# Kernel tuning notes

Hardware: AMD Instinct MI355X
Metric: run time of the kernel (lower is better)

## Reference

```python
import jax, jax.numpy as jnp
import numpy as np

HIDDEN = 2048
HEADS = 16
HEAD_DIM = HIDDEN // HEADS
BATCH = 2
SEQ = 2048


def setup_inputs() -> dict:
    key = jax.random.key(0)
    ks = jax.random.split(key, 9)
    s = 0.02
    return {
        "x": jax.random.normal(ks[0], (BATCH, SEQ, HIDDEN), dtype=jnp.float32),
        "wq": jax.random.normal(ks[1], (HIDDEN, HIDDEN), dtype=jnp.float32) * s,
        "bq": jax.random.normal(ks[2], (HIDDEN,), dtype=jnp.float32) * s,
        "wk": jax.random.normal(ks[3], (HIDDEN, HIDDEN), dtype=jnp.float32) * s,
        "bk": jax.random.normal(ks[4], (HIDDEN,), dtype=jnp.float32) * s,
        "wv": jax.random.normal(ks[5], (HIDDEN, HIDDEN), dtype=jnp.float32) * s,
        "bv": jax.random.normal(ks[6], (HIDDEN,), dtype=jnp.float32) * s,
        "wo": jax.random.normal(ks[7], (HIDDEN, HIDDEN), dtype=jnp.float32) * s,
        "bo": jax.random.normal(ks[8], (HIDDEN,), dtype=jnp.float32) * s,
    }


def reference(x, wq, bq, wk, bk, wv, bv, wo, bo):
    B, S, _ = x.shape
    scale = jnp.sqrt(jnp.float32(HEAD_DIM))
    # torch Linear: y = x @ W.T + b
    def proj(w, b):
        return (x @ w.T + b).reshape(B, S, HEADS, HEAD_DIM).transpose(0, 2, 1, 3)
    q = proj(wq, bq)  # [B,H,S,D]
    k = proj(wk, bk)
    v = proj(wv, bv)
    scores = jnp.einsum("bhqd,bhkd->bhqk", q, k) / scale  # [B,H,S,S]
    probs = jax.nn.softmax(scores, axis=-1)
    ctx = jnp.einsum("bhqk,bhkd->bhqd", probs, v)  # [B,H,S,D]
    ctx = ctx.transpose(0, 2, 1, 3).reshape(B, S, HIDDEN)
    return ctx @ wo.T + bo
```

## Files before the change

kernel.cpp:

```cpp
#include <hip/hip_runtime.h>

typedef unsigned short u16;
typedef unsigned int   u32;
typedef float  f32x4   __attribute__((ext_vector_type(4)));
typedef __bf16 bf16x8  __attribute__((ext_vector_type(8)));
typedef u16    u16x8   __attribute__((ext_vector_type(8)));
typedef u16    u16x4   __attribute__((ext_vector_type(4)));
typedef u32    u32x2   __attribute__((ext_vector_type(2)));
typedef u32    u32x4   __attribute__((ext_vector_type(4)));

#define HIDDEN 2048
#define SEQ    2048
#define NHEADS 16
#define HD     128
#define BATCH  2
#define QSTR   4096

typedef const __attribute__((address_space(3))) u16* lptr;

__device__ __forceinline__ u16 f2bf(float f) {
  u32 u = __builtin_bit_cast(u32, f);
  u += 0x7FFFu + ((u >> 16) & 1u);
  return (u16)(u >> 16);
}
__device__ __forceinline__ u32 pk2(float a, float b) {
  __bf16 x = (__bf16)a, y = (__bf16)b;
  return (u32)__builtin_bit_cast(u16, x) | ((u32)__builtin_bit_cast(u16, y) << 16);
}
__device__ __forceinline__ bf16x8 ld_frag(const u16* p) {
  return __builtin_bit_cast(bf16x8, *(const u32x4*)p);
}
__device__ __forceinline__ void gload_lds16(const u16* g, u16* l) {
  __builtin_amdgcn_global_load_lds((const __attribute__((address_space(1))) u32*)g,
                                   (__attribute__((address_space(3))) u32*)l, 16, 0, 0);
}

#define DSR(dst, base, lit) \
  asm volatile("ds_read_b128 %0, %1 offset:" lit : "=v"(dst) : "v"(base))

#define MFMA16(d, a, b) d = __builtin_amdgcn_mfma_f32_16x16x32_bf16(a, b, d, 0, 0, 0)

__global__ __launch_bounds__(256) void cvt_kernel(const float* __restrict__ src,
                                                  u16* __restrict__ dst, int n4) {
  int stride = gridDim.x * blockDim.x;
  for (int i = blockIdx.x * blockDim.x + threadIdx.x; i < n4; i += stride) {
    f32x4 v = ((const f32x4*)src)[i];
    u16x4 o;
    o[0] = f2bf(v[0]); o[1] = f2bf(v[1]); o[2] = f2bf(v[2]); o[3] = f2bf(v[3]);
    *(u16x4*)(dst + (size_t)i * 4) = o;
  }
}

__global__ __launch_bounds__(256) void cvt4_kernel(
    const float* __restrict__ s0, const float* __restrict__ s1,
    const float* __restrict__ s2, const float* __restrict__ s3,
    u16* __restrict__ o0, u16* __restrict__ o1,
    u16* __restrict__ o2, u16* __restrict__ o3, int n4) {
  const float* src = (blockIdx.y == 0) ? s0 : (blockIdx.y == 1) ? s1 : (blockIdx.y == 2) ? s2 : s3;
  u16* dst = (blockIdx.y == 0) ? o0 : (blockIdx.y == 1) ? o1 : (blockIdx.y == 2) ? o2 : o3;
  int stride = gridDim.x * blockDim.x;
  for (int i = blockIdx.x * blockDim.x + threadIdx.x; i < n4; i += stride) {
    f32x4 v = ((const f32x4*)src)[i];
    u16x4 o;
    o[0] = f2bf(v[0]); o[1] = f2bf(v[1]); o[2] = f2bf(v[2]); o[3] = f2bf(v[3]);
    *(u16x4*)(dst + (size_t)i * 4) = o;
  }
}

__global__ __launch_bounds__(512, 2) void gemm_qkv(
    const u16* __restrict__ A, const u16* __restrict__ Bt,
    const float* __restrict__ bq, const float* __restrict__ bk,
    const float* __restrict__ bv,
    u16* __restrict__ qk, u16* __restrict__ vtb, float qscale)
{
  __shared__ __attribute__((aligned(16))) u16 As[2][16384];
  __shared__ __attribute__((aligned(16))) u16 Bs[2][12288];

  const int tid  = threadIdx.x;
  const int lane = tid & 63;
  const int wave = tid >> 6;
  const int l15  = lane & 15;
  const int g    = lane >> 4;
  const int wm   = wave >> 2;
  const int wn   = wave & 3;

  const int id  = blockIdx.x;
  const int xcd = id & 7;
  const int c   = id >> 3;
  const int tileN = (xcd * 4 + (c >> 4)) * 192;
  const int tileM = (c & 15) << 8;

  const int srow = tid >> 3;
  const int gch8 = ((tid & 7) ^ (srow & 7)) * 8;
  const u16* agp = A  + (size_t)(tileM + srow) * HIDDEN + gch8;
  const u16* bgp = Bt + (size_t)(tileN + srow) * HIDDEN + gch8;
  u16* asp = (u16*)&As[0][0] + tid * 8;
  u16* bsp = (u16*)&Bs[0][0] + tid * 8;

  auto stage = [&](int buf, int ko) {
    u16* ad = asp + buf * 16384;
    u16* bd = bsp + buf * 12288;
#pragma unroll
    for (int r = 0; r < 4; ++r)
      gload_lds16(agp + (size_t)r * 64 * HIDDEN + ko, ad + r * 4096);
#pragma unroll
    for (int r = 0; r < 3; ++r)
      gload_lds16(bgp + (size_t)r * 64 * HIDDEN + ko, bd + r * 4096);
  };

  const int sw = l15 & 7;
  const int c0 = (g ^ sw) * 8;
  const int c1 = ((g ^ sw) ^ 4) * 8;
  lptr aT = (lptr)&As[0][0] + (size_t)(wm * 128 + l15) * 64;
  lptr bT = (lptr)&Bs[0][0] + (size_t)(wn * 48 + l15) * 64;

  f32x4 acc[8][3] = {};
  bf16x8 Xa[8], Xb[3], Ya[8], Yb[3];

#define ISSUE_SET(Sa, Sb, ab, bb)      \
  DSR(Sa[0], ab, "0");                 \
  DSR(Sa[1], ab, "2048");              \
  DSR(Sa[2], ab, "4096");              \
  DSR(Sa[3], ab, "6144");              \
  DSR(Sb[0], bb, "0");                 \
  DSR(Sb[1], bb, "2048");              \
  DSR(Sb[2], bb, "4096");              \
  DSR(Sa[4], ab, "8192");              \
  DSR(Sa[5], ab, "10240");             \
  DSR(Sa[6], ab, "12288");             \
  DSR(Sa[7], ab, "14336");

#define MFMA12A(Sa, Sb)                                                                   \
  _Pragma("unroll")                                                                       \
  for (int mf = 0; mf < 4; ++mf) {                                                        \
    _Pragma("unroll")                                                                     \
    for (int nf = 0; nf < 3; ++nf)                                                        \
      acc[mf][nf] = __builtin_amdgcn_mfma_f32_16x16x32_bf16(Sa[mf], Sb[nf], acc[mf][nf], 0, 0, 0); \
  }
#define MFMA12B(Sa, Sb)                                                                   \
  _Pragma("unroll")                                                                       \
  for (int mf = 4; mf < 8; ++mf) {                                                        \
    _Pragma("unroll")                                                                     \
    for (int nf = 0; nf < 3; ++nf)                                                        \
      acc[mf][nf] = __builtin_amdgcn_mfma_f32_16x16x32_bf16(Sa[mf], Sb[nf], acc[mf][nf], 0, 0, 0); \
  }

  stage(0, 0);
  stage(1, 64);
  asm volatile("s_waitcnt vmcnt(7)" ::: "memory");
  __builtin_amdgcn_s_barrier();
  __builtin_amdgcn_sched_barrier(0);
  {
    lptr ab = aT + c0;
    lptr bb = bT + c0;
    ISSUE_SET(Xa, Xb, ab, bb)
  }

#pragma unroll 2
  for (int t = 0; t < 32; ++t) {
    const int cur = t & 1;
    {
      lptr ab = aT + cur * 16384 + c1;
      lptr bb = bT + cur * 12288 + c1;
      ISSUE_SET(Ya, Yb, ab, bb)
    }
    asm volatile("s_waitcnt lgkmcnt(15)" ::: "memory");
    __builtin_amdgcn_sched_barrier(0);
    __builtin_amdgcn_s_setprio(1);
    MFMA12A(Xa, Xb)
    __builtin_amdgcn_s_setprio(0);
    __builtin_amdgcn_sched_barrier(0);
    asm volatile("s_waitcnt lgkmcnt(11)" ::: "memory");
    __builtin_amdgcn_sched_barrier(0);
    __builtin_amdgcn_s_setprio(1);
    MFMA12B(Xa, Xb)
    __builtin_amdgcn_s_setprio(0);
    __builtin_amdgcn_sched_barrier(0);
    asm volatile("s_waitcnt lgkmcnt(4)" ::: "memory");
    __builtin_amdgcn_sched_barrier(0);
    __builtin_amdgcn_s_setprio(1);
    MFMA12A(Ya, Yb)
    __builtin_amdgcn_s_setprio(0);
    __builtin_amdgcn_sched_barrier(0);
    asm volatile("s_waitcnt lgkmcnt(0)" ::: "memory");
    __builtin_amdgcn_sched_barrier(0);
    __builtin_amdgcn_s_barrier();
    __builtin_amdgcn_sched_barrier(0);
    if (t < 30) stage(cur, (t + 2) * 64);
    __builtin_amdgcn_sched_barrier(0);
    if (t < 30) {
      asm volatile("s_waitcnt vmcnt(7)" ::: "memory");
    } else {
      asm volatile("s_waitcnt vmcnt(0)" ::: "memory");
    }
    __builtin_amdgcn_s_barrier();
    __builtin_amdgcn_sched_barrier(0);
    if (t < 31) {
      lptr ab = aT + (cur ^ 1) * 16384 + c0;
      lptr bb = bT + (cur ^ 1) * 12288 + c0;
      ISSUE_SET(Xa, Xb, ab, bb)
    }
    __builtin_amdgcn_sched_barrier(0);
    __builtin_amdgcn_s_setprio(1);
    MFMA12B(Ya, Yb)
    __builtin_amdgcn_s_setprio(0);
    __builtin_amdgcn_sched_barrier(0);
  }

#pragma unroll
  for (int mi = 0; mi < 8; ++mi) {
#pragma unroll
    for (int ni = 0; ni < 3; ++ni) {
      const int gcb = tileN + wn * 48 + ni * 16;
      const int seg = gcb >> 11;
      const int gc  = gcb + l15;
      const float bvv = ((seg == 0) ? bq : (seg == 1) ? bk : bv)[gc & 2047];
      if (seg < 2) {
        const float scl = (seg == 0) ? qscale : 1.f;
#pragma unroll
        for (int j = 0; j < 4; ++j) {
          const int gr = tileM + wm * 128 + mi * 16 + g * 4 + j;
          qk[(size_t)gr * QSTR + gc] = f2bf((acc[mi][ni][j] + bvv) * scl);
        }
      } else {
        const int dglob = gc - 4096;
        const int hh = dglob >> 7, dd = dglob & 127;
        const int srow0 = tileM + wm * 128 + mi * 16 + g * 4;
        const int bb = srow0 >> 11, ss = srow0 & 2047;
        u16x4 o;
#pragma unroll
        for (int j = 0; j < 4; ++j) o[j] = f2bf(acc[mi][ni][j] + bvv);
        *(u16x4*)(vtb + ((size_t)((bb * NHEADS + hh) * HD + dd)) * SEQ + ss) = o;
      }
    }
  }
#undef ISSUE_SET
#undef MFMA12A
#undef MFMA12B
}

__global__ __launch_bounds__(512, 2) void gemm_o(
    const u16* __restrict__ A, const u16* __restrict__ Bt,
    const float* __restrict__ bias, float* __restrict__ Cout)
{
  __shared__ __attribute__((aligned(16))) u16 As[2][16384];
  __shared__ __attribute__((aligned(16))) u16 Bs[2][8192];

  const int tid  = threadIdx.x;
  const int lane = tid & 63;
  const int wave = tid >> 6;
  const int l15  = lane & 15;
  const int g    = lane >> 4;
  const int wm   = wave >> 1;
  const int wn   = wave & 1;

  const int id  = blockIdx.x;
  const int xcd = id & 7;
  const int c   = id >> 3;
  const int tileN = (xcd * 2 + (c >> 4)) << 7;
  const int tileM = (c & 15) << 8;

  const int sr   = tid >> 3;
  const int sgc  = ((tid & 7) ^ (sr & 7)) * 8;
  const u16* agp = A  + (size_t)(tileM + sr) * HIDDEN + sgc;
  const u16* bgp = Bt + (size_t)(tileN + sr) * HIDDEN + sgc;
  u16* asp = (u16*)&As[0][0] + tid * 8;
  u16* bsp = (u16*)&Bs[0][0] + tid * 8;

  auto stage = [&](int buf, int ko) {
    u16* ad = asp + buf * 16384;
    u16* bd = bsp + buf * 8192;
#pragma unroll
    for (int r = 0; r < 4; ++r)
      gload_lds16(agp + (size_t)r * 64 * HIDDEN + ko, ad + r * 4096);
#pragma unroll
    for (int r = 0; r < 2; ++r)
      gload_lds16(bgp + (size_t)r * 64 * HIDDEN + ko, bd + r * 4096);
  };

  const int sw = l15 & 7;
  const int c0 = (g ^ sw) * 8;
  const int c1 = ((g ^ sw) ^ 4) * 8;
  lptr aT = (lptr)&As[0][0] + (size_t)(wm * 64 + l15) * 64;
  lptr bT = (lptr)&Bs[0][0] + (size_t)(wn * 64 + l15) * 64;

  f32x4 acc[4][4] = {};
  bf16x8 Xa[4], Xb[4], Ya[4], Yb[4];

#define ISSUE8O(Sa, Sb, ab, bb) \
  DSR(Sa[0], ab, "0"); DSR(Sa[1], ab, "2048"); DSR(Sa[2], ab, "4096"); DSR(Sa[3], ab, "6144"); \
  DSR(Sb[0], bb, "0"); DSR(Sb[1], bb, "2048"); DSR(Sb[2], bb, "4096"); DSR(Sb[3], bb, "6144");

#define MFMA16O(Sa, Sb)                                                                   \
  _Pragma("unroll")                                                                       \
  for (int mf = 0; mf < 4; ++mf) {                                                        \
    _Pragma("unroll")                                                                     \
    for (int nf = 0; nf < 4; ++nf)                                                        \
      acc[mf][nf] = __builtin_amdgcn_mfma_f32_16x16x32_bf16(Sa[mf], Sb[nf], acc[mf][nf], 0, 0, 0); \
  }

  stage(0, 0);
  stage(1, 64);
  asm volatile("s_waitcnt vmcnt(6)" ::: "memory");
  __builtin_amdgcn_s_barrier();
  __builtin_amdgcn_sched_barrier(0);
  {
    lptr ab = aT + c0;
    lptr bb = bT + c0;
    ISSUE8O(Xa, Xb, ab, bb)
  }

#pragma unroll 2
  for (int t = 0; t < 32; ++t) {
    const int cur = t & 1;
    {
      lptr ab = aT + cur * 16384 + c1;
      lptr bb = bT + cur * 8192 + c1;
      ISSUE8O(Ya, Yb, ab, bb)
    }
    asm volatile("s_waitcnt lgkmcnt(8)" ::: "memory");
    __builtin_amdgcn_sched_barrier(0);
    __builtin_amdgcn_s_setprio(1);
    MFMA16O(Xa, Xb)
    __builtin_amdgcn_s_setprio(0);
    asm volatile("s_waitcnt lgkmcnt(0)" ::: "memory");
    __builtin_amdgcn_sched_barrier(0);
    __builtin_amdgcn_s_barrier();
    __builtin_amdgcn_sched_barrier(0);
    if (t < 30) stage(cur, (t + 2) * 64);
    __builtin_amdgcn_sched_barrier(0);
    __builtin_amdgcn_s_setprio(1);
    MFMA16O(Ya, Yb)
    __builtin_amdgcn_s_setprio(0);
    __builtin_amdgcn_sched_barrier(0);
    if (t < 30) {
      asm volatile("s_waitcnt vmcnt(6)" ::: "memory");
    } else {
      asm volatile("s_waitcnt vmcnt(0)" ::: "memory");
    }
    __builtin_amdgcn_s_barrier();
    __builtin_amdgcn_sched_barrier(0);
    if (t < 31) {
      lptr ab = aT + (cur ^ 1) * 16384 + c0;
      lptr bb = bT + (cur ^ 1) * 8192 + c0;
      ISSUE8O(Xa, Xb, ab, bb)
    }
  }
#undef ISSUE8O
#undef MFMA16O

#pragma unroll
  for (int mf = 0; mf < 4; ++mf) {
#pragma unroll
    for (int nf = 0; nf < 4; ++nf) {
      const int gc = tileN + wn * 64 + nf * 16 + l15;
      const float bv = bias[gc];
#pragma unroll
      for (int j = 0; j < 4; ++j) {
        const int gr = tileM + wm * 64 + mf * 16 + g * 4 + j;
        Cout[(size_t)gr * HIDDEN + gc] = acc[mf][nf][j] + bv;
      }
    }
  }
}

__global__ __launch_bounds__(256, 2) void attn_kernel(
    const u16* __restrict__ QKg, const u16* __restrict__ Vtg, u16* __restrict__ Ctx)
{
  __shared__ __attribute__((aligned(16))) u16 Ks[2][64 * 128];
  __shared__ __attribute__((aligned(16))) u16 Vs[2][128 * 64];

  const int tid  = threadIdx.x;
  const int lane = tid & 63;
  const int wave = tid >> 6;
  const int g4   = lane >> 4;
  const int l15  = lane & 15;

  const int wg = ((blockIdx.x & 7) << 6) + (blockIdx.x >> 3);
  const int bh = wg >> 4;
  const int qt = wg & 15;
  const int b  = bh >> 4, h = bh & 15;

  const u16* Qb  = QKg + (size_t)b * SEQ * QSTR + (size_t)h * HD;
  const u16* Kb  = Qb + 2048;
  const u16* Vth = Vtg + (size_t)bh * HD * SEQ;
  u16* Cb = Ctx + (size_t)b * SEQ * HIDDEN + (size_t)h * HD;

  const int qbase = qt * 128 + wave * 32 + l15;

  bf16x8 qf[2][4];
#pragma unroll
  for (int qs = 0; qs < 2; qs++)
#pragma unroll
    for (int dc = 0; dc < 4; dc++)
      qf[qs][dc] = ld_frag(Qb + (size_t)(qbase + qs * 16) * QSTR + dc * 32 + g4 * 8);

  const int kvp0 = (l15 >> 2) * 8 + (l15 & 3);
  const int msw  = (l15 & 3) | (((l15 >> 2) & 1) << 2);
  const int msw3 = msw & 3;
  const int mk   = (l15 >> 2) & 1;
  const int kcol = (g4 ^ msw3) * 8;

  lptr ksb = (lptr)&Ks[0][0];
  lptr kE0 = ksb + (kvp0      ) * 128 + kcol + mk * 32;
  lptr kO0 = ksb + (kvp0      ) * 128 + kcol + (1 ^ mk) * 32;
  lptr kE1 = ksb + (kvp0 +   4) * 128 + kcol + mk * 32;
  lptr kO1 = ksb + (kvp0 +   4) * 128 + kcol + (1 ^ mk) * 32;
  lptr kE2 = ksb + (kvp0 +  32) * 128 + kcol + mk * 32;
  lptr kO2 = ksb + (kvp0 +  32) * 128 + kcol + (1 ^ mk) * 32;
  lptr kE3 = ksb + (kvp0 +  36) * 128 + kcol + mk * 32;
  lptr kO3 = ksb + (kvp0 +  36) * 128 + kcol + (1 ^ mk) * 32;

  lptr vsb = (lptr)&Vs[0][0];
  lptr vB0 = vsb + l15 * 64 + ((0 * 4 + g4) ^ (l15 & 7)) * 8;
  lptr vB1 = vsb + l15 * 64 + ((1 * 4 + g4) ^ (l15 & 7)) * 8;

  const u16* kg[4];
  const u16* vg[4];
  u16* ksd = (u16*)&Ks[0][0] + tid * 8;
  u16* vsd = (u16*)&Vs[0][0] + tid * 8;
#pragma unroll
  for (int i = 0; i < 4; i++) {
    const int idx = tid + i * 256;
    const int kv = idx >> 4, up = idx & 15;
    const int um = up ^ ((kv & 3) | (((kv >> 3) & 1) << 2));
    kg[i] = Kb + (size_t)kv * QSTR + um * 8;
    const int d = idx >> 3, u = idx & 7;
    const int uv = u ^ (d & 7);
    vg[i] = Vth + (size_t)d * SEQ + uv * 8;
  }

  auto stage = [&](int buf, int kv0) {
    u16* kd = ksd + buf * 8192;
    u16* vd = vsd + buf * 8192;
#pragma unroll
    for (int i = 0; i < 4; i++) gload_lds16(kg[i] + (size_t)kv0 * QSTR, kd + i * 2048);
#pragma unroll
    for (int i = 0; i < 4; i++) gload_lds16(vg[i] + kv0, vd + i * 2048);
  };

  f32x4 ctx[2][8] = {};
  float m_run[2] = {-1e30f, -1e30f};
  float l_run[2] = {0.f, 0.f};

  stage(0, 0);

  const int NT = SEQ / 64;
  for (int t = 0; t < NT; t++) {
    const int buf = t & 1;

    if (t + 1 < NT) {
      stage(buf ^ 1, (t + 1) * 64);
      asm volatile("s_waitcnt vmcnt(8)" ::: "memory");
    } else {
      asm volatile("s_waitcnt vmcnt(0)" ::: "memory");
    }
    __builtin_amdgcn_s_barrier();
    __builtin_amdgcn_sched_barrier(0);

    bf16x8 kf[4][4];
    {
      const int bo = buf * 8192;
      lptr e0 = kE0 + bo, o0 = kO0 + bo, e1 = kE1 + bo, o1 = kO1 + bo;
      lptr e2 = kE2 + bo, o2 = kO2 + bo, e3 = kE3 + bo, o3 = kO3 + bo;
      DSR(kf[0][0], e0, "0"); DSR(kf[0][1], o0, "0"); DSR(kf[0][2], e0, "128"); DSR(kf[0][3], o0, "128");
      DSR(kf[1][0], e1, "0"); DSR(kf[1][1], o1, "0"); DSR(kf[1][2], e1, "128"); DSR(kf[1][3], o1, "128");
      DSR(kf[2][0], e2, "0"); DSR(kf[2][1], o2, "0"); DSR(kf[2][2], e2, "128"); DSR(kf[2][3], o2, "128");
      DSR(kf[3][0], e3, "0"); DSR(kf[3][1], o3, "0"); DSR(kf[3][2], e3, "128"); DSR(kf[3][3], o3, "128");
    }
    f32x4 s[2][4] = {};
    asm volatile("s_waitcnt lgkmcnt(8)" ::: "memory");
    __builtin_amdgcn_sched_barrier(0);
    __builtin_amdgcn_s_setprio(1);
#pragma unroll
    for (int ni = 0; ni < 2; ni++)
#pragma unroll
      for (int dc = 0; dc < 4; dc++) {
        MFMA16(s[0][ni], kf[ni][dc], qf[0][dc]);
        MFMA16(s[1][ni], kf[ni][dc], qf[1][dc]);
      }
    __builtin_amdgcn_sched_barrier(0);
    asm volatile("s_waitcnt lgkmcnt(0)" ::: "memory");
    __builtin_amdgcn_sched_barrier(0);
#pragma unroll
    for (int ni = 2; ni < 4; ni++)
#pragma unroll
      for (int dc = 0; dc < 4; dc++) {
        MFMA16(s[0][ni], kf[ni][dc], qf[0][dc]);
        MFMA16(s[1][ni], kf[ni][dc], qf[1][dc]);
      }
    __builtin_amdgcn_s_setprio(0);
    __builtin_amdgcn_sched_barrier(0);

    float pmax[2];
#pragma unroll
    for (int qs = 0; qs < 2; qs++) {
      float m0 = fmaxf(fmaxf(s[qs][0][0], s[qs][0][1]), fmaxf(s[qs][0][2], s[qs][0][3]));
      float m1 = fmaxf(fmaxf(s[qs][1][0], s[qs][1][1]), fmaxf(s[qs][1][2], s[qs][1][3]));
      float m2 = fmaxf(fmaxf(s[qs][2][0], s[qs][2][1]), fmaxf(s[qs][2][2], s[qs][2][3]));
      float m3 = fmaxf(fmaxf(s[qs][3][0], s[qs][3][1]), fmaxf(s[qs][3][2], s[qs][3][3]));
      pmax[qs] = fmaxf(fmaxf(m0, m1), fmaxf(m2, m3));
      pmax[qs] = fmaxf(pmax[qs], __shfl_xor(pmax[qs], 16));
      pmax[qs] = fmaxf(pmax[qs], __shfl_xor(pmax[qs], 32));
    }
    const bool ok0 = (pmax[0] <= m_run[0] + 8.f);
    const bool ok1 = (pmax[1] <= m_run[1] + 8.f);
    if (!__all(ok0 && ok1)) {
#pragma unroll
      for (int qs = 0; qs < 2; qs++) {
        const float mn = fmaxf(m_run[qs], pmax[qs]);
        const float corr = exp2f(m_run[qs] - mn);
        m_run[qs] = mn;
        l_run[qs] *= corr;
#pragma unroll
        for (int dt = 0; dt < 8; dt++)
#pragma unroll
          for (int j = 0; j < 4; j++) ctx[qs][dt][j] *= corr;
      }
    }
    bf16x8 pfrag[2][2];
#pragma unroll
    for (int qs = 0; qs < 2; qs++) {
      float ps = 0.f;
#pragma unroll
      for (int ni = 0; ni < 4; ni++)
#pragma unroll
        for (int j = 0; j < 4; j++) {
          const float p = exp2f(s[qs][ni][j] - m_run[qs]);
          s[qs][ni][j] = p;
          ps += p;
        }
      l_run[qs] += ps;
#pragma unroll
      for (int hh = 0; hh < 2; hh++) {
        u32x4 pw;
        pw[0] = pk2(s[qs][2 * hh][0], s[qs][2 * hh][1]);
        pw[1] = pk2(s[qs][2 * hh][2], s[qs][2 * hh][3]);
        pw[2] = pk2(s[qs][2 * hh + 1][0], s[qs][2 * hh + 1][1]);
        pw[3] = pk2(s[qs][2 * hh + 1][2], s[qs][2 * hh + 1][3]);
        pfrag[qs][hh] = __builtin_bit_cast(bf16x8, pw);
      }
    }
    __builtin_amdgcn_sched_barrier(0);

    bf16x8 vf[2][8];
    {
      lptr v0 = vB0 + buf * 8192;
      lptr v1 = vB1 + buf * 8192;
      DSR(vf[0][0], v0, "0");     DSR(vf[0][1], v0, "2048");
      DSR(vf[0][2], v0, "4096");  DSR(vf[0][3], v0, "6144");
      DSR(vf[0][4], v0, "8192");  DSR(vf[0][5], v0, "10240");
      DSR(vf[0][6], v0, "12288"); DSR(vf[0][7], v0, "14336");
      DSR(vf[1][0], v1, "0");     DSR(vf[1][1], v1, "2048");
      DSR(vf[1][2], v1, "4096");  DSR(vf[1][3], v1, "6144");
      DSR(vf[1][4], v1, "8192");  DSR(vf[1][5], v1, "10240");
      DSR(vf[1][6], v1, "12288"); DSR(vf[1][7], v1, "14336");
    }
    asm volatile("s_waitcnt lgkmcnt(8)" ::: "memory");
    __builtin_amdgcn_sched_barrier(0);
    __builtin_amdgcn_s_setprio(1);
#pragma unroll
    for (int dt = 0; dt < 8; dt++) {
      MFMA16(ctx[0][dt], vf[0][dt], pfrag[0][0]);
      MFMA16(ctx[1][dt], vf[0][dt], pfrag[1][0]);
    }
    __builtin_amdgcn_sched_barrier(0);
    asm volatile("s_waitcnt lgkmcnt(0)" ::: "memory");
    __builtin_amdgcn_sched_barrier(0);
#pragma unroll
    for (int dt = 0; dt < 8; dt++) {
      MFMA16(ctx[0][dt], vf[1][dt], pfrag[0][1]);
      MFMA16(ctx[1][dt], vf[1][dt], pfrag[1][1]);
    }
    __builtin_amdgcn_s_setprio(0);
    __builtin_amdgcn_sched_barrier(0);

    __builtin_amdgcn_s_barrier();
    __builtin_amdgcn_sched_barrier(0);
  }

#pragma unroll
  for (int qs = 0; qs < 2; qs++) {
    float lt = l_run[qs];
    lt += __shfl_xor(lt, 16);
    lt += __shfl_xor(lt, 32);
    const float linv = 1.f / lt;
    u16* crow = Cb + (size_t)(qbase + qs * 16) * HIDDEN;
#pragma unroll
    for (int dt = 0; dt < 8; dt++) {
      u16x4 o;
#pragma unroll
      for (int j = 0; j < 4; j++) o[j] = f2bf(ctx[qs][dt][j] * linv);
      *(u16x4*)&crow[dt * 16 + g4 * 4] = o;
    }
  }
}

extern "C" void kernel_launch(void* const* d_in, const int* in_sizes, int n_in,
                              void* d_out, int out_size, void* d_ws, size_t ws_size,
                              hipStream_t stream) {
  (void)in_sizes; (void)n_in; (void)out_size; (void)ws_size;
  const float* x  = (const float*)d_in[0];
  const float* wq = (const float*)d_in[1];
  const float* bq = (const float*)d_in[2];
  const float* wk = (const float*)d_in[3];
  const float* bk = (const float*)d_in[4];
  const float* wv = (const float*)d_in[5];
  const float* bv = (const float*)d_in[6];
  const float* wo = (const float*)d_in[7];
  const float* bo = (const float*)d_in[8];

  const size_t NX = (size_t)BATCH * SEQ * HIDDEN;
  const size_t NW = (size_t)HIDDEN * HIDDEN;
  u16* xb   = (u16*)d_ws;
  u16* wqb  = xb  + NX;
  u16* wkb  = wqb + NW;
  u16* wvb  = wkb + NW;
  u16* wob  = wvb + NW;
  u16* qk   = wob + NW;
  u16* vtb  = qk  + 2 * NX;
  u16* ctxb = xb;

  cvt_kernel<<<2048, 256, 0, stream>>>(x, xb, (int)(NX / 4));
  cvt4_kernel<<<dim3(512, 4), 256, 0, stream>>>(wq, wk, wv, wo, wqb, wkb, wvb, wob, (int)(NW / 4));

  const float qscale = 0.12751744174240807f;
  gemm_qkv<<<512, 512, 0, stream>>>(xb, wqb, bq, bk, bv, qk, vtb, qscale);

  attn_kernel<<<512, 256, 0, stream>>>(qk, vtb, ctxb);

  gemm_o<<<256, 512, 0, stream>>>(ctxb, wob, bo, (float*)d_out);
}
```

Measured before the change: 253.9 us.

## Restructure QKV GEMM into four-slot 32-wide K pipeline with phased barriers

The QKV projection GEMM moves from a double-buffered 64-wide K tile to four LDS slots of 32-wide K, with a new XOR swizzle and fragment addressing. Global-to-LDS loads are issued one half-tile at a time, and each iteration is split into four barrier-delimited MFMA phases with per-wave vmcnt waits. The aim is to overlap global loads with MFMA work more finely and shorten exposed LDS-read latency. In exchange it adds more barriers per K step and more complex wait-count bookkeeping, so a wrong count could produce a race.

```diff
diff --git a/kernel.cpp b/kernel.cpp
--- a/kernel.cpp
+++ b/kernel.cpp
@@ -73,8 +73,8 @@
     const float* __restrict__ bv,
     u16* __restrict__ qk, u16* __restrict__ vtb, float qscale)
 {
-  __shared__ __attribute__((aligned(16))) u16 As[2][16384];
-  __shared__ __attribute__((aligned(16))) u16 Bs[2][12288];
+  __shared__ __attribute__((aligned(16))) u16 As[4][8192];
+  __shared__ __attribute__((aligned(16))) u16 Bs[4][6144];
 
   const int tid  = threadIdx.x;
   const int lane = tid & 63;
@@ -90,45 +90,32 @@
   const int tileN = (xcd * 4 + (c >> 4)) * 192;
   const int tileM = (c & 15) << 8;
 
-  const int srow = tid >> 3;
-  const int gch8 = ((tid & 7) ^ (srow & 7)) * 8;
-  const u16* agp = A  + (size_t)(tileM + srow) * HIDDEN + gch8;
-  const u16* bgp = Bt + (size_t)(tileN + srow) * HIDDEN + gch8;
-  u16* asp = (u16*)&As[0][0] + tid * 8;
-  u16* bsp = (u16*)&Bs[0][0] + tid * 8;
-
-  auto stage = [&](int buf, int ko) {
-    u16* ad = asp + buf * 16384;
-    u16* bd = bsp + buf * 12288;
-#pragma unroll
-    for (int r = 0; r < 4; ++r)
-      gload_lds16(agp + (size_t)r * 64 * HIDDEN + ko, ad + r * 4096);
-#pragma unroll
-    for (int r = 0; r < 3; ++r)
-      gload_lds16(bgp + (size_t)r * 64 * HIDDEN + ko, bd + r * 4096);
+  const int ra  = tid >> 2;
+  const int ca  = (tid & 3) ^ ((ra >> 1) & 3);
+  const u16* agp = A  + (size_t)(tileM + ra) * HIDDEN + ca * 8;
+  const u16* bgp = Bt + (size_t)(tileN + ra) * HIDDEN + ca * 8;
+
+  auto stage = [&](int sl, int ko) {
+    u16* ad = (u16*)&As[0][0] + sl * 8192 + tid * 8;
+    u16* bd = (u16*)&Bs[0][0] + sl * 6144 + tid * 8;
+    gload_lds16(agp + ko, ad);
+    gload_lds16(agp + (size_t)128 * HIDDEN + ko, ad + 4096);
+    gload_lds16(bgp + ko, bd);
+    if (tid < 256) gload_lds16(bgp + (size_t)128 * HIDDEN + ko, bd + 4096);
   };
 
-  const int sw = l15 & 7;
-  const int c0 = (g ^ sw) * 8;
-  const int c1 = ((g ^ sw) ^ 4) * 8;
-  lptr aT = (lptr)&As[0][0] + (size_t)(wm * 128 + l15) * 64;
-  lptr bT = (lptr)&Bs[0][0] + (size_t)(wn * 48 + l15) * 64;
+  const int fk = (g ^ ((l15 >> 1) & 3)) * 8;
+  lptr aT = (lptr)&As[0][0] + (size_t)(wm * 128 + l15) * 32 + fk;
+  lptr bT = (lptr)&Bs[0][0] + (size_t)(wn * 48 + l15) * 32 + fk;
 
   f32x4 acc[8][3] = {};
   bf16x8 Xa[8], Xb[3], Ya[8], Yb[3];
 
-#define ISSUE_SET(Sa, Sb, ab, bb)      \
-  DSR(Sa[0], ab, "0");                 \
-  DSR(Sa[1], ab, "2048");              \
-  DSR(Sa[2], ab, "4096");              \
-  DSR(Sa[3], ab, "6144");              \
-  DSR(Sb[0], bb, "0");                 \
-  DSR(Sb[1], bb, "2048");              \
-  DSR(Sb[2], bb, "4096");              \
-  DSR(Sa[4], ab, "8192");              \
-  DSR(Sa[5], ab, "10240");             \
-  DSR(Sa[6], ab, "12288");             \
-  DSR(Sa[7], ab, "14336");
+#define RD7(Sa, Sb, ab, bb) \
+  DSR(Sa[0], ab, "0"); DSR(Sa[1], ab, "1024"); DSR(Sa[2], ab, "2048"); DSR(Sa[3], ab, "3072"); \
+  DSR(Sb[0], bb, "0"); DSR(Sb[1], bb, "1024"); DSR(Sb[2], bb, "2048");
+#define RD4(Sa, ab) \
+  DSR(Sa[4], ab, "4096"); DSR(Sa[5], ab, "5120"); DSR(Sa[6], ab, "6144"); DSR(Sa[7], ab, "7168");
 
 #define MFMA12A(Sa, Sb)                                                                   \
   _Pragma("unroll")                                                                       \
@@ -145,66 +132,51 @@
       acc[mf][nf] = __builtin_amdgcn_mfma_f32_16x16x32_bf16(Sa[mf], Sb[nf], acc[mf][nf], 0, 0, 0); \
   }
 
+#define VMW(nlo, nhi) \
+  if (wave < 4) { asm volatile("s_waitcnt vmcnt(" #nlo ")" ::: "memory"); } \
+  else          { asm volatile("s_waitcnt vmcnt(" #nhi ")" ::: "memory"); }
+
+#define PHASE_TAIL(MF)                                  \
+  __builtin_amdgcn_s_barrier();                         \
+  asm volatile("s_waitcnt lgkmcnt(0)" ::: "memory");    \
+  __builtin_amdgcn_sched_barrier(0);                    \
+  __builtin_amdgcn_s_setprio(1);                        \
+  MF                                                    \
+  __builtin_amdgcn_s_setprio(0);                        \
+  __builtin_amdgcn_s_barrier();                         \
+  __builtin_amdgcn_sched_barrier(0);
+
   stage(0, 0);
-  stage(1, 64);
-  asm volatile("s_waitcnt vmcnt(7)" ::: "memory");
+  stage(1, 32);
+  stage(2, 64);
+  VMW(8, 6)
   __builtin_amdgcn_s_barrier();
   __builtin_amdgcn_sched_barrier(0);
-  {
-    lptr ab = aT + c0;
-    lptr bb = bT + c0;
-    ISSUE_SET(Xa, Xb, ab, bb)
-  }
 
 #pragma unroll 2
   for (int t = 0; t < 32; ++t) {
-    const int cur = t & 1;
-    {
-      lptr ab = aT + cur * 16384 + c1;
-      lptr bb = bT + cur * 12288 + c1;
-      ISSUE_SET(Ya, Yb, ab, bb)
-    }
-    asm volatile("s_waitcnt lgkmcnt(15)" ::: "memory");
-    __builtin_amdgcn_sched_barrier(0);
-    __builtin_amdgcn_s_setprio(1);
-    MFMA12A(Xa, Xb)
-    __builtin_amdgcn_s_setprio(0);
-    __builtin_amdgcn_sched_barrier(0);
-    asm volatile("s_waitcnt lgkmcnt(11)" ::: "memory");
-    __builtin_amdgcn_sched_barrier(0);
-    __builtin_amdgcn_s_setprio(1);
-    MFMA12B(Xa, Xb)
-    __builtin_amdgcn_s_setprio(0);
-    __builtin_amdgcn_sched_barrier(0);
-    asm volatile("s_waitcnt lgkmcnt(4)" ::: "memory");
-    __builtin_amdgcn_sched_barrier(0);
-    __builtin_amdgcn_s_setprio(1);
-    MFMA12A(Ya, Yb)
-    __builtin_amdgcn_s_setprio(0);
-    __builtin_amdgcn_sched_barrier(0);
-    asm volatile("s_waitcnt lgkmcnt(0)" ::: "memory");
-    __builtin_amdgcn_sched_barrier(0);
-    __builtin_amdgcn_s_barrier();
-    __builtin_amdgcn_sched_barrier(0);
-    if (t < 30) stage(cur, (t + 2) * 64);
-    __builtin_amdgcn_sched_barrier(0);
-    if (t < 30) {
-      asm volatile("s_waitcnt vmcnt(7)" ::: "memory");
-    } else {
-      asm volatile("s_waitcnt vmcnt(0)" ::: "memory");
-    }
-    __builtin_amdgcn_s_barrier();
-    __builtin_amdgcn_sched_barrier(0);
-    if (t < 31) {
-      lptr ab = aT + (cur ^ 1) * 16384 + c0;
-      lptr bb = bT + (cur ^ 1) * 12288 + c0;
-      ISSUE_SET(Xa, Xb, ab, bb)
-    }
-    __builtin_amdgcn_sched_barrier(0);
-    __builtin_amdgcn_s_setprio(1);
-    MFMA12B(Ya, Yb)
-    __builtin_amdgcn_s_setprio(0);
-    __builtin_amdgcn_sched_barrier(0);
+    const int s0 = (2 * t) & 3, s1 = s0 + 1;
+    lptr a0 = aT + s0 * 8192, b0 = bT + s0 * 6144;
+    lptr a1 = aT + s1 * 8192, b1 = bT + s1 * 6144;
+
+    RD7(Xa, Xb, a0, b0)
+    if (t < 31) stage(s1 ^ 2, (t + 1) * 64 + 32);
+    PHASE_TAIL(MFMA12A(Xa, Xb))
+
+    RD4(Xa, a0)
+    if (t == 31) { asm volatile("s_waitcnt vmcnt(0)" ::: "memory"); }
+    else         { VMW(8, 6) }
+    PHASE_TAIL(MFMA12B(Xa, Xb))
+
+    RD7(Ya, Yb, a1, b1)
+    if (t < 30) stage(s0, (t + 2) * 64);
+    PHASE_TAIL(MFMA12A(Ya, Yb))
+
+    RD4(Ya, a1)
+    if (t < 30)      { VMW(8, 6) }
+    else if (t == 30){ VMW(4, 3) }
+    else             { asm volatile("s_waitcnt vmcnt(0)" ::: "memory"); }
+    PHASE_TAIL(MFMA12B(Ya, Yb))
   }
 
 #pragma unroll
@@ -234,9 +206,12 @@
       }
     }
   }
-#undef ISSUE_SET
+#undef RD7
+#undef RD4
 #undef MFMA12A
 #undef MFMA12B
+#undef VMW
+#undef PHASE_TAIL
 }
 
 __global__ __launch_bounds__(512, 2) void gemm_o(
```

Result: slower. 261.2 us (+2.9%).
